# Performance work log

Hardware: AMD Instinct MI355X
Metric: run time of the kernel (lower is better)

## Reference

```python
import jax, jax.numpy as jnp
import numpy as np

TEMPORAL_LAMBDA = 0.1


def setup_inputs() -> dict:
    key = jax.random.key(0)
    k1, k2 = jax.random.split(key)
    preds = jax.random.normal(k1, (2, 8, 16, 128, 256), dtype=jnp.float32)   # (B,T,M,H,W)
    target = jax.random.normal(k2, (2, 8, 1, 128, 256), dtype=jnp.float32)   # (B,T,1,H,W)
    return {"preds": preds, "target": target}


def reference(preds, target):
    # CRPS = E[|X - y|] - 0.5 * E[|X - X'|]
    term1 = jnp.abs(preds - target).mean(axis=2)                 # (B,T,H,W)
    # pairwise |x_i - x_j| over ensemble dim (M x M broadcast, as in original)
    pairwise = jnp.abs(preds[:, :, :, None] - preds[:, :, None, :])  # (B,T,M,M,H,W)
    term2 = 0.5 * pairwise.mean(axis=(2, 3))                     # (B,T,H,W)
    crps = term1 - term2
    # temporal consistency penalty (temporal_lambda > 0 branch)
    crps = crps.mean(axis=1)                                     # (B,H,W)
    temporal_diff = preds[:, 1:] - preds[:, :-1]                 # (B,T-1,M,H,W)
    temporal_penalty = jnp.abs(temporal_diff).mean(axis=(1, 2))  # (B,H,W)
    crps = crps + TEMPORAL_LAMBDA * temporal_penalty
    crps = crps[:, None, None]                                   # (B,1,1,H,W)
    return crps.mean()                                           # reduction='mean'
```

## Files before the change

kernel.cpp:

```cpp
#include <hip/hip_runtime.h>

#define HW    32768
#define T_DIM 8
#define E_DIM 16
#define NPOS  65536
#define BLK   256
#define NTHREADS 262144
#define NBLK  (NTHREADS / BLK)

__device__ __forceinline__ float block_reduce_256(float v, float* lds) {
#pragma unroll
    for (int off = 32; off; off >>= 1)
        v += __shfl_down(v, off, 64);
    int lane = threadIdx.x & 63;
    int wid  = threadIdx.x >> 6;
    if (lane == 0) lds[wid] = v;
    __syncthreads();
    return lds[0] + lds[1] + lds[2] + lds[3];
}

__device__ __forceinline__ float crps_term(const float* p, float tgt) {
    float t1 = 0.f;
#pragma unroll
    for (int e = 0; e < E_DIM; ++e)
        t1 += fabsf(p[e] - tgt);
    float s = 0.f;
#pragma unroll
    for (int i = 0; i < E_DIM; ++i)
#pragma unroll
        for (int j = i + 1; j < E_DIM; ++j)
            s += fabsf(p[i] - p[j]);
    return t1 * (1.f / 16.f) - s * (1.f / 256.f);
}

__global__ __launch_bounds__(BLK) void crps_partial(const float* __restrict__ preds,
                                                    const float* __restrict__ target,
                                                    float* __restrict__ partials) {
    const int n  = blockIdx.x * BLK + threadIdx.x;
    const int k  = n & 3;
    const int hw = (n >> 2) & (HW - 1);
    const int b  = n >> 17;
    const int t0 = 2 * k;

    const float* pb = preds  + hw;
    const float* tb = target + hw;

    float cur0[E_DIM], cur1[E_DIM];
#pragma unroll
    for (int e = 0; e < E_DIM; ++e)
        cur0[e] = pb[((size_t)((b * T_DIM + t0) * E_DIM) + e) * HW];
#pragma unroll
    for (int e = 0; e < E_DIM; ++e)
        cur1[e] = pb[((size_t)((b * T_DIM + t0 + 1) * E_DIM) + e) * HW];
    const float tgt0 = tb[(size_t)(b * T_DIM + t0) * HW];
    const float tgt1 = tb[(size_t)(b * T_DIM + t0 + 1) * HW];

    const int lane = threadIdx.x & 63;
    const int src  = (lane > 0) ? (lane - 1) : 0;
    float tacc = 0.f;
#pragma unroll
    for (int e = 0; e < E_DIM; ++e) {
        float pv = __shfl(cur1[e], src, 64);
        if (k > 0)
            tacc += fabsf(cur0[e] - pv);
    }
#pragma unroll
    for (int e = 0; e < E_DIM; ++e)
        tacc += fabsf(cur1[e] - cur0[e]);

    float acc = crps_term(cur0, tgt0) + crps_term(cur1, tgt1);

    float v = acc * (1.f / 8.f) + tacc * (0.1f / 112.f);

    __shared__ float lds[4];
    float bsum = block_reduce_256(v, lds);
    if (threadIdx.x == 0)
        partials[blockIdx.x] = bsum;
}

__global__ __launch_bounds__(BLK) void crps_final(const float* __restrict__ partials,
                                                  float* __restrict__ out) {
    float v = 0.f;
#pragma unroll
    for (int i = 0; i < NBLK / BLK; ++i)
        v += partials[i * BLK + threadIdx.x];
    __shared__ float lds[4];
    float total = block_reduce_256(v, lds);
    if (threadIdx.x == 0)
        out[0] = total * (1.f / (float)NPOS);
}

extern "C" void kernel_launch(void* const* d_in, const int* in_sizes, int n_in,
                              void* d_out, int out_size, void* d_ws, size_t ws_size,
                              hipStream_t stream) {
    const float* preds  = (const float*)d_in[0];
    const float* target = (const float*)d_in[1];
    float* out      = (float*)d_out;
    float* partials = (float*)d_ws;

    crps_partial<<<NBLK, BLK, 0, stream>>>(preds, target, partials);
    crps_final<<<1, BLK, 0, stream>>>(partials, out);
}
```

Before: 13.48 us.

## Replace O(M^2) pairwise abs sum with sorting network and rank-weighted sum

The ensemble pairwise absolute-difference sum is computed by sorting the 16 members with a min/max sorting network and summing rank-weighted differences, instead of all 120 pair terms. This cuts per-thread ALU work for the second CRPS term. The sort overwrites the register arrays in place, so the target term is computed first, and the network adds register shuffling.

```diff
diff --git a/kernel.cpp b/kernel.cpp
--- a/kernel.cpp
+++ b/kernel.cpp
@@ -19,18 +19,41 @@
     return lds[0] + lds[1] + lds[2] + lds[3];
 }
 
-__device__ __forceinline__ float crps_term(const float* p, float tgt) {
-    float t1 = 0.f;
-#pragma unroll
-    for (int e = 0; e < E_DIM; ++e)
-        t1 += fabsf(p[e] - tgt);
-    float s = 0.f;
-#pragma unroll
-    for (int i = 0; i < E_DIM; ++i)
-#pragma unroll
-        for (int j = i + 1; j < E_DIM; ++j)
-            s += fabsf(p[i] - p[j]);
-    return t1 * (1.f / 16.f) - s * (1.f / 256.f);
+__device__ __forceinline__ void ce(float& a, float& b) {
+    float lo = fminf(a, b);
+    float hi = fmaxf(a, b);
+    a = lo; b = hi;
+}
+
+__device__ __forceinline__ float pairsum_destructive(float* x) {
+    ce(x[0],x[1]);  ce(x[2],x[3]);  ce(x[4],x[5]);   ce(x[6],x[7]);
+    ce(x[8],x[9]);  ce(x[10],x[11]); ce(x[12],x[13]); ce(x[14],x[15]);
+    ce(x[0],x[2]);  ce(x[1],x[3]);  ce(x[4],x[6]);   ce(x[5],x[7]);
+    ce(x[8],x[10]); ce(x[9],x[11]); ce(x[12],x[14]); ce(x[13],x[15]);
+    ce(x[1],x[2]);  ce(x[5],x[6]);  ce(x[9],x[10]);  ce(x[13],x[14]);
+    ce(x[0],x[4]);  ce(x[1],x[5]);  ce(x[2],x[6]);   ce(x[3],x[7]);
+    ce(x[8],x[12]); ce(x[9],x[13]); ce(x[10],x[14]); ce(x[11],x[15]);
+    ce(x[2],x[4]);  ce(x[3],x[5]);  ce(x[10],x[12]); ce(x[11],x[13]);
+    ce(x[1],x[2]);  ce(x[3],x[4]);  ce(x[5],x[6]);
+    ce(x[9],x[10]); ce(x[11],x[12]); ce(x[13],x[14]);
+    ce(x[0],x[8]);  ce(x[1],x[9]);  ce(x[2],x[10]);  ce(x[3],x[11]);
+    ce(x[4],x[12]); ce(x[5],x[13]); ce(x[6],x[14]);  ce(x[7],x[15]);
+    ce(x[4],x[8]);  ce(x[5],x[9]);  ce(x[6],x[10]);  ce(x[7],x[11]);
+    ce(x[2],x[4]);  ce(x[3],x[5]);  ce(x[6],x[8]);
+    ce(x[7],x[9]);  ce(x[10],x[12]); ce(x[11],x[13]);
+    ce(x[1],x[2]);  ce(x[3],x[4]);  ce(x[5],x[6]);   ce(x[7],x[8]);
+    ce(x[9],x[10]); ce(x[11],x[12]); ce(x[13],x[14]);
+
+    float s;
+    s  = 15.f * (x[15] - x[0]);
+    s += 13.f * (x[14] - x[1]);
+    s += 11.f * (x[13] - x[2]);
+    s +=  9.f * (x[12] - x[3]);
+    s +=  7.f * (x[11] - x[4]);
+    s +=  5.f * (x[10] - x[5]);
+    s +=  3.f * (x[9]  - x[6]);
+    s +=         x[8]  - x[7];
+    return s;
 }
 
 __global__ __launch_bounds__(BLK) void crps_partial(const float* __restrict__ preds,
@@ -68,7 +91,15 @@
     for (int e = 0; e < E_DIM; ++e)
         tacc += fabsf(cur1[e] - cur0[e]);
 
-    float acc = crps_term(cur0, tgt0) + crps_term(cur1, tgt1);
+    float t1 = 0.f;
+#pragma unroll
+    for (int e = 0; e < E_DIM; ++e)
+        t1 += fabsf(cur0[e] - tgt0) + fabsf(cur1[e] - tgt1);
+
+    float s0 = pairsum_destructive(cur0);
+    float s1 = pairsum_destructive(cur1);
+
+    float acc = t1 * (1.f / 16.f) - (s0 + s1) * (1.f / 256.f);
 
     float v = acc * (1.f / 8.f) + tacc * (0.1f / 112.f);
 
```

Result: slower. 13.99 us (+3.8%).
